# Kernel optimization log

Measured on AMD Instinct MI355X. Metric: run time of the kernel, lower is better.

Reference implementation:

```python
import jax, jax.numpy as jnp
import numpy as np

N_ITER = 25
TOP_G = 0.07
BOT_G = 0.07
N_MIX = 1.0  # n=1 -> top target is exactly global_target


def _conv(x, W, b, stride):
    # NCHW valid conv, matching torch Conv2d
    y = jax.lax.conv_general_dilated(
        x, W, (stride, stride), 'VALID',
        dimension_numbers=('NCHW', 'OIHW', 'NCHW'))
    return y + b[None, :, None, None]


def setup_inputs() -> dict:
    key = jax.random.key(0)
    ks = jax.random.split(key, 8)
    B = 2048
    x = jax.random.normal(ks[0], (B, 3, 32, 32), jnp.float32)
    global_target = jax.random.uniform(ks[1], (B, 10), jnp.float32)

    def he(k, shape, fan_in):
        return jax.random.normal(k, shape, jnp.float32) * (1.0 / np.sqrt(fan_in))

    W1 = he(ks[2], (64, 3, 5, 5), 3 * 25);    b1 = jnp.zeros((64,), jnp.float32)
    W2 = he(ks[3], (128, 64, 5, 5), 64 * 25); b2 = jnp.zeros((128,), jnp.float32)
    W3 = he(ks[4], (256, 128, 3, 3), 128 * 9); b3 = jnp.zeros((256,), jnp.float32)
    W4 = he(ks[5], (10, 1024), 1024);          b4 = jnp.zeros((10,), jnp.float32)
    return {"x": x, "global_target": global_target,
            "W1": W1, "b1": b1, "W2": W2, "b2": b2,
            "W3": W3, "b3": b3, "W4": W4, "b4": b4}


def reference(x, global_target, W1, b1, W2, b2, W3, b3, W4, b4):
    B = x.shape[0]
    # layer functions (wts[0..3] in the torch module)
    f1 = lambda z: jax.nn.relu(_conv(z, W1, b1, 2))                      # [B,64,14,14]
    f2 = lambda z: jax.nn.relu(_conv(z, W2, b2, 2))                      # [B,128,5,5]
    f3 = lambda z: jax.nn.relu(_conv(z, W3, b3, 2)).reshape(z.shape[0], -1)  # [B,1024]
    f4 = lambda z: z @ W4.T + b4                                         # [B,10]

    # compute_values: feedforward pass
    h1 = f1(x); h2 = f2(h1); h3 = f3(h2); h4 = f4(h3)
    # top target: n*global_target + (1-n)*h4  (n=1)
    t4 = N_MIX * global_target + (1.0 - N_MIX) * h4

    # compute_PC_targets: iterative inference.
    # p[1] = wts[0](targ[0]) = f1(x) is constant == h1, so eps1 = t1 - h1.
    def step(carry, _):
        t1, t2, t3, p2, p3, p4 = carry
        e1 = t1 - h1
        e2 = t2 - p2
        e3 = t3 - p3
        e4 = (t4 - jax.nn.softmax(p4, axis=1)) * 0.5
        # epsdfdt = vjp of next layer at current target, cotangent = next eps
        _, v2 = jax.vjp(f2, t1); (g1,) = v2(e2)
        _, v3 = jax.vjp(f3, t2); (g2,) = v3(e3)
        _, v4 = jax.vjp(f4, t3); (g3,) = v4(e4)
        t1 = t1 + TOP_G * (-e1) + BOT_G * g1
        t2 = t2 + TOP_G * (-e2) + BOT_G * g2
        t3 = t3 + TOP_G * (-e3) + BOT_G * g3
        # recompute predictions from updated targets
        p2 = f2(t1); p3 = f3(t2); p4 = f4(t3)
        return (t1, t2, t3, p2, p3, p4), None

    carry0 = (h1, h2, h3, h2, h3, h4)
    (t1, t2, t3, _, _, _), _ = jax.lax.scan(step, carry0, None, length=N_ITER)

    # return refined PC targets (targ[1..3]; targ[0]=x and targ[4]=global_target are fixed)
    return jnp.concatenate(
        [t1.reshape(B, -1), t2.reshape(B, -1), t3.reshape(B, -1)], axis=1)
```

## Files before the change

kernel.cpp:

```cpp
#include <hip/hip_runtime.h>
#include <hip/hip_bf16.h>

typedef __hip_bfloat16 bf16;
typedef __attribute__((ext_vector_type(8))) short short8v;
typedef __attribute__((ext_vector_type(4))) float float4v;


__device__ __forceinline__ float b2f(bf16 v) { return __bfloat162float(v); }
__device__ __forceinline__ bf16  f2b(float v) { return __float2bfloat16(v); }
__device__ __forceinline__ float blo(unsigned u) { return __uint_as_float(u << 16); }
__device__ __forceinline__ float bhi(unsigned u) { return __uint_as_float(u & 0xffff0000u); }
__device__ __forceinline__ unsigned short fbits(float v) {
  union { bf16 b; unsigned short u; } c; c.b = f2b(v); return c.u;
}
__device__ __forceinline__ float ubf(unsigned short u) {
  return __uint_as_float(((unsigned)u) << 16);
}
__device__ __forceinline__ void gld16(const void* g, void* l) {
  __builtin_amdgcn_global_load_lds((const unsigned int*)g, (unsigned int*)l, 16, 0, 0);
}

__global__ __launch_bounds__(256) void k_prep(
    const float* __restrict__ W1, const float* __restrict__ W2,
    const float* __restrict__ W3, float* __restrict__ W1t,
    short* __restrict__ W2f, short* __restrict__ W2u,
    short* __restrict__ W3m, short* __restrict__ W3u) {
  int i = blockIdx.x * 256 + threadIdx.x;
  if (i < 4800) {
    int oc = i / 75, k = i % 75;
    W1t[k * 64 + oc] = W1[i];
  }
  if (i < 204800) {
    int oc = i / 1600, k = i % 1600, ic = k / 25, tap = k % 25;
    float w = W2[i];
    unsigned short hi = fbits(w);
    unsigned short lo = fbits(w - ubf(hi));
    W2f[(tap * 128 + oc) * 64 + (ic ^ ((oc & 7) << 3))] = (short)hi;
    W2f[204800 + (tap * 128 + oc) * 64 + (ic ^ ((oc & 7) << 3))] = (short)lo;
    W2u[(tap * 64 + ic) * 128 + (oc ^ ((ic & 7) << 3))] = (short)hi;
  }
  if (i < 294912) {
    int oc = i / 1152, k = i % 1152, ic = k / 9, tap = k % 9;
    float w = W3[i];
    unsigned short hi = fbits(w);
    unsigned short lo = fbits(w - ubf(hi));
    W3m[(tap * 256 + oc) * 128 + (ic ^ ((oc & 7) << 3))] = (short)hi;
    W3m[294912 + (tap * 256 + oc) * 128 + (ic ^ ((oc & 7) << 3))] = (short)lo;
    W3u[(tap * 128 + ic) * 256 + (oc ^ ((ic & 7) << 3))] = (short)hi;
  }
}

__global__ __launch_bounds__(512, 1) void k_conv1s(
    const float* __restrict__ x, const float* __restrict__ W1t,
    const float* __restrict__ b1, bf16* __restrict__ h1T) {
  __shared__ float xs[480 * 66];
  __shared__ float ws[4800];
  int bt = blockIdx.x, oy = blockIdx.y;
  int tid = threadIdx.x, lane = tid & 63, w8 = tid >> 6;
  int wv = w8 & 3, h = w8 >> 2;
  for (int i = tid; i < 4800; i += 512) ws[i] = W1t[i];
#pragma unroll
  for (int r = 0; r < 15; ++r) {
    int idx = r * 512 + tid;
    int col = idx / 120, q = idx % 120;
    int ic = q / 40, rem = q % 40;
    float4 v = *(const float4*)(x + (size_t)(bt * 64 + col) * 3072 +
                                ic * 1024 + oy * 64 + rem * 4);
    float* d = xs + (ic * 160 + rem * 4) * 66 + col;
    d[0] = v.x;
    d[66] = v.y;
    d[132] = v.z;
    d[198] = v.w;
  }
  __syncthreads();
  int oc0 = wv * 16;
  float acc[7][16];
#pragma unroll
  for (int o = 0; o < 7; ++o)
#pragma unroll
    for (int j = 0; j < 16; ++j) acc[o][j] = b1[oc0 + j];
  for (int ic = 0; ic < 3; ++ic)
    for (int ky = 0; ky < 5; ++ky) {
#pragma unroll
      for (int kx = 0; kx < 5; ++kx) {
        const float* wp = ws + ((ic * 25 + ky * 5 + kx) << 6) + oc0;
        float4 w0 = *(const float4*)(wp);
        float4 w1 = *(const float4*)(wp + 4);
        float4 w2 = *(const float4*)(wp + 8);
        float4 w3 = *(const float4*)(wp + 12);
        const float* xr = xs + (ic * 160 + ky * 32 + kx) * 66 + lane;
        float xv[7];
#pragma unroll
        for (int o = 0; o < 7; ++o) xv[o] = xr[(2 * (h * 7 + o)) * 66];
#pragma unroll
        for (int o = 0; o < 7; ++o) {
          float e = xv[o];
          acc[o][0] += e * w0.x;  acc[o][1] += e * w0.y;
          acc[o][2] += e * w0.z;  acc[o][3] += e * w0.w;
          acc[o][4] += e * w1.x;  acc[o][5] += e * w1.y;
          acc[o][6] += e * w1.z;  acc[o][7] += e * w1.w;
          acc[o][8] += e * w2.x;  acc[o][9] += e * w2.y;
          acc[o][10] += e * w2.z; acc[o][11] += e * w2.w;
          acc[o][12] += e * w3.x; acc[o][13] += e * w3.y;
          acc[o][14] += e * w3.z; acc[o][15] += e * w3.w;
        }
      }
    }
#pragma unroll
  for (int o = 0; o < 7; ++o) {
    int pix = oy * 14 + h * 7 + o;
    size_t tbase = ((size_t)(pix * 32 + bt)) << 12;
#pragma unroll
    for (int q = 0; q < 4; ++q) {
      ushort4 pk;
      pk.x = fbits(fmaxf(acc[o][q * 4 + 0], 0.f));
      pk.y = fbits(fmaxf(acc[o][q * 4 + 1], 0.f));
      pk.z = fbits(fmaxf(acc[o][q * 4 + 2], 0.f));
      pk.w = fbits(fmaxf(acc[o][q * 4 + 3], 0.f));
      int ocr = oc0 + q * 4;
      size_t off = tbase + lane * 64 + (ocr ^ ((lane & 7) << 3));
      *(ushort4*)(h1T + off) = pk;
    }
  }
}

__global__ __launch_bounds__(256) void k_fwd2m(
    const bf16* __restrict__ in1, const short* __restrict__ W2f,
    const float* __restrict__ b2, bf16* __restrict__ p2T,
    const bf16* __restrict__ t2e, bf16* __restrict__ e2T, int einit) {
  __shared__ __align__(16) short As0[8192];
  __shared__ __align__(16) short As1[8192];
  __shared__ __align__(16) short Bs[2][4096];
  int bid = blockIdx.x;
  int j = bid >> 3;
  int cbp = (bid & 7) * 2 + (j & 1), pos = j >> 1;
  int cb0 = cbp * 2;
  int tid = threadIdx.x, lane = tid & 63, wv = tid >> 6;
  int oy = pos / 5, ox = pos % 5;
  float4v acc[2][2][4];
#pragma unroll
  for (int c = 0; c < 2; ++c)
#pragma unroll
    for (int m = 0; m < 2; ++m)
#pragma unroll
      for (int n = 0; n < 4; ++n) acc[c][m][n] = (float4v){0.f, 0.f, 0.f, 0.f};

  for (int tap = 0; tap < 25; ++tap) {
    int ky = tap / 5, kx = tap % 5;
    int ipix = (2 * oy + ky) * 14 + (2 * ox + kx);
    __syncthreads();
    {
      const uint4* bs0 = (const uint4*)(in1 + (((size_t)(ipix * 32 + cb0)) << 12));
      const uint4* bs1 = (const uint4*)(in1 + (((size_t)(ipix * 32 + cb0 + 1)) << 12));
      uint4* bd = (uint4*)Bs;
      gld16(&bs0[tid], &bd[tid]);
      gld16(&bs0[tid + 256], &bd[tid + 256]);
      gld16(&bs1[tid], &bd[tid + 512]);
      gld16(&bs1[tid + 256], &bd[tid + 768]);
      const uint4* ah = (const uint4*)(W2f + tap * 8192);
      const uint4* al = (const uint4*)(W2f + 204800 + tap * 8192);
      uint4* dh = (uint4*)As0;
      uint4* dl = (uint4*)As1;
#pragma unroll
      for (int p = 0; p < 4; ++p) {
        gld16(&ah[tid + p * 256], &dh[tid + p * 256]);
        gld16(&al[tid + p * 256], &dl[tid + p * 256]);
      }
    }
    __syncthreads();
#pragma unroll
    for (int ks = 0; ks < 2; ++ks) {
      int ic0 = ks * 32 + ((lane >> 4) << 3);
      short8v bfr[2][4];
#pragma unroll
      for (int c = 0; c < 2; ++c)
#pragma unroll
        for (int n = 0; n < 4; ++n) {
          int colv = n * 16 + (lane & 15);
          bfr[c][n] = *(const short8v*)(&Bs[c][0] + colv * 64 + (ic0 ^ ((colv & 7) << 3)));
        }
#pragma unroll
      for (int m = 0; m < 2; ++m) {
        int row = wv * 32 + m * 16 + (lane & 15);
        int aoff = row * 64 + (ic0 ^ ((row & 7) << 3));
        short8v ah = *(const short8v*)(As0 + aoff);
        short8v al = *(const short8v*)(As1 + aoff);
#pragma unroll
        for (int c = 0; c < 2; ++c)
#pragma unroll
          for (int n = 0; n < 4; ++n) {
            acc[c][m][n] = __builtin_amdgcn_mfma_f32_16x16x32_bf16(ah, bfr[c][n], acc[c][m][n], 0, 0, 0);
            acc[c][m][n] = __builtin_amdgcn_mfma_f32_16x16x32_bf16(al, bfr[c][n], acc[c][m][n], 0, 0, 0);
          }
      }
    }
  }
#pragma unroll
  for (int c = 0; c < 2; ++c) {
    size_t tb2 = ((size_t)(pos * 32 + cb0 + c)) << 13;
#pragma unroll
    for (int m = 0; m < 2; ++m) {
      int ocb = wv * 32 + m * 16 + ((lane >> 4) << 2);
      float4 bv = *(const float4*)(b2 + ocb);
#pragma unroll
      for (int n = 0; n < 4; ++n) {
        int colv = n * 16 + (lane & 15);
        ushort4 pk;
        pk.x = fbits(fmaxf(acc[c][m][n][0] + bv.x, 0.f));
        pk.y = fbits(fmaxf(acc[c][m][n][1] + bv.y, 0.f));
        pk.z = fbits(fmaxf(acc[c][m][n][2] + bv.z, 0.f));
        pk.w = fbits(fmaxf(acc[c][m][n][3] + bv.w, 0.f));
        size_t off = tb2 + colv * 128 + (ocb ^ ((colv & 7) << 3));
        *(ushort4*)(p2T + off) = pk;
        if (einit) {
          ushort4 z = {0, 0, 0, 0};
          *(ushort4*)(e2T + off) = z;
        } else {
          ushort4 tv = *(const ushort4*)(t2e + off);
          ushort4 ev;
          float p0, t0;
          p0 = ubf(pk.x); t0 = ubf(tv.x); ev.x = fbits(p0 > 0.f ? t0 - p0 : 0.f);
          p0 = ubf(pk.y); t0 = ubf(tv.y); ev.y = fbits(p0 > 0.f ? t0 - p0 : 0.f);
          p0 = ubf(pk.z); t0 = ubf(tv.z); ev.z = fbits(p0 > 0.f ? t0 - p0 : 0.f);
          p0 = ubf(pk.w); t0 = ubf(tv.w); ev.w = fbits(p0 > 0.f ? t0 - p0 : 0.f);
          *(ushort4*)(e2T + off) = ev;
        }
      }
    }
  }
}

__global__ __launch_bounds__(256) void k_upd1m(
    const bf16* __restrict__ e2T, const short* __restrict__ W2u,
    const bf16* __restrict__ h1T, const bf16* __restrict__ t1r,
    bf16* __restrict__ t1w) {
  __shared__ __align__(16) short As0[8192];
  __shared__ __align__(16) short Es[2][8192];
  int bid = blockIdx.x;
  int j = bid >> 3;
  int cbp = (bid & 7) * 2 + (j & 1), pix = j >> 1;
  int cb0 = cbp * 2;
  int tid = threadIdx.x, lane = tid & 63, wv = tid >> 6;
  int iy = pix / 14, ix = pix % 14;
  float4v acc[2][4];
#pragma unroll
  for (int c = 0; c < 2; ++c)
#pragma unroll
    for (int n = 0; n < 4; ++n) acc[c][n] = (float4v){0.f, 0.f, 0.f, 0.f};

  for (int ky = iy & 1; ky <= 4; ky += 2) {
    int oy = (iy - ky) >> 1;
    if (oy < 0 || oy > 4) continue;
    for (int kx = ix & 1; kx <= 4; kx += 2) {
      int ox = (ix - kx) >> 1;
      if (ox < 0 || ox > 4) continue;
      int erow = oy * 5 + ox, tap = ky * 5 + kx;
      __syncthreads();
      {
        const uint4* es0 = (const uint4*)(e2T + (((size_t)(erow * 32 + cb0)) << 13));
        const uint4* es1 = (const uint4*)(e2T + (((size_t)(erow * 32 + cb0 + 1)) << 13));
        uint4* ed = (uint4*)Es;
        const uint4* ah = (const uint4*)(W2u + tap * 8192);
        uint4* dh = (uint4*)As0;
#pragma unroll
        for (int p = 0; p < 4; ++p) {
          gld16(&es0[tid + p * 256], &ed[tid + p * 256]);
          gld16(&es1[tid + p * 256], &ed[tid + p * 256 + 1024]);
          gld16(&ah[tid + p * 256], &dh[tid + p * 256]);
        }
      }
      __syncthreads();
#pragma unroll
      for (int ks = 0; ks < 4; ++ks) {
        int oc0 = ks * 32 + ((lane >> 4) << 3);
        int row = wv * 16 + (lane & 15);
        int aoff = row * 128 + (oc0 ^ ((row & 7) << 3));
        short8v ah = *(const short8v*)(As0 + aoff);
#pragma unroll
        for (int c = 0; c < 2; ++c)
#pragma unroll
          for (int n = 0; n < 4; ++n) {
            int colv = n * 16 + (lane & 15);
            short8v ef = *(const short8v*)(&Es[c][0] + colv * 128 + (oc0 ^ ((colv & 7) << 3)));
            acc[c][n] = __builtin_amdgcn_mfma_f32_16x16x32_bf16(ah, ef, acc[c][n], 0, 0, 0);
          }
      }
    }
  }
  int icb = wv * 16 + ((lane >> 4) << 2);
#pragma unroll
  for (int c = 0; c < 2; ++c) {
    size_t tb1 = ((size_t)(pix * 32 + cb0 + c)) << 12;
#pragma unroll
    for (int n = 0; n < 4; ++n) {
      int colv = n * 16 + (lane & 15);
      size_t off = tb1 + colv * 64 + (icb ^ ((colv & 7) << 3));
      ushort4 tv = *(const ushort4*)(t1r + off);
      ushort4 hv = *(const ushort4*)(h1T + off);
      ushort4 rp;
      float t0, h0;
      t0 = ubf(tv.x); h0 = ubf(hv.x);
      rp.x = fbits(t0 - 0.07f * (t0 - h0) + 0.07f * acc[c][n][0]);
      t0 = ubf(tv.y); h0 = ubf(hv.y);
      rp.y = fbits(t0 - 0.07f * (t0 - h0) + 0.07f * acc[c][n][1]);
      t0 = ubf(tv.z); h0 = ubf(hv.z);
      rp.z = fbits(t0 - 0.07f * (t0 - h0) + 0.07f * acc[c][n][2]);
      t0 = ubf(tv.w); h0 = ubf(hv.w);
      rp.w = fbits(t0 - 0.07f * (t0 - h0) + 0.07f * acc[c][n][3]);
      *(ushort4*)(t1w + off) = rp;
    }
  }
}

__global__ __launch_bounds__(256) void k_fwd3m(
    const bf16* __restrict__ in2, const short* __restrict__ W3m,
    const float* __restrict__ b3, bf16* __restrict__ p3T,
    const bf16* __restrict__ t3e, bf16* __restrict__ e3T, int einit) {
  __shared__ __align__(16) short As0[8192];
  __shared__ __align__(16) short As1[8192];
  __shared__ __align__(16) short Bs[8192];
  int bid = blockIdx.x;
  int j = bid >> 3;
  int cb = (bid & 7) * 4 + (j & 3);
  int r = j >> 2;
  int pos = r & 3, och = r >> 2;
  int tid = threadIdx.x, lane = tid & 63, wv = tid >> 6;
  int oy = pos >> 1, ox = pos & 1;
  float4v acc[4];
#pragma unroll
  for (int n = 0; n < 4; ++n) acc[n] = (float4v){0.f, 0.f, 0.f, 0.f};

  for (int tap = 0; tap < 9; ++tap) {
    int ky = tap / 3, kx = tap % 3;
    int irow = (2 * oy + ky) * 5 + (2 * ox + kx);
    __syncthreads();
    {
      const uint4* bs = (const uint4*)(in2 + (((size_t)(irow * 32 + cb)) << 13));
      uint4* bd = (uint4*)Bs;
#pragma unroll
      for (int p = 0; p < 4; ++p) gld16(&bs[tid + p * 256], &bd[tid + p * 256]);
      const uint4* ah = (const uint4*)(W3m + ((size_t)tap * 256 + och * 64) * 128);
      const uint4* al = (const uint4*)(W3m + 294912 + ((size_t)tap * 256 + och * 64) * 128);
      uint4* dh = (uint4*)As0;
      uint4* dl = (uint4*)As1;
#pragma unroll
      for (int p = 0; p < 4; ++p) {
        gld16(&ah[tid + p * 256], &dh[tid + p * 256]);
        gld16(&al[tid + p * 256], &dl[tid + p * 256]);
      }
    }
    __syncthreads();
#pragma unroll
    for (int ks = 0; ks < 4; ++ks) {
      int ic0 = ks * 32 + ((lane >> 4) << 3);
      short8v bfr[4];
#pragma unroll
      for (int n = 0; n < 4; ++n) {
        int colv = n * 16 + (lane & 15);
        bfr[n] = *(const short8v*)(Bs + colv * 128 + (ic0 ^ ((colv & 7) << 3)));
      }
      int row = wv * 16 + (lane & 15);
      int aoff = row * 128 + (ic0 ^ ((row & 7) << 3));
      short8v ah = *(const short8v*)(As0 + aoff);
      short8v al = *(const short8v*)(As1 + aoff);
#pragma unroll
      for (int n = 0; n < 4; ++n) {
        acc[n] = __builtin_amdgcn_mfma_f32_16x16x32_bf16(ah, bfr[n], acc[n], 0, 0, 0);
        acc[n] = __builtin_amdgcn_mfma_f32_16x16x32_bf16(al, bfr[n], acc[n], 0, 0, 0);
      }
    }
  }
  size_t tb3 = ((size_t)(pos * 32 + cb)) << 14;
  int ocg = och * 64 + wv * 16 + ((lane >> 4) << 2);
  float4 bv = *(const float4*)(b3 + ocg);
#pragma unroll
  for (int n = 0; n < 4; ++n) {
    int colv = n * 16 + (lane & 15);
    ushort4 pk;
    pk.x = fbits(fmaxf(acc[n][0] + bv.x, 0.f));
    pk.y = fbits(fmaxf(acc[n][1] + bv.y, 0.f));
    pk.z = fbits(fmaxf(acc[n][2] + bv.z, 0.f));
    pk.w = fbits(fmaxf(acc[n][3] + bv.w, 0.f));
    size_t off = tb3 + colv * 256 + (ocg ^ ((colv & 7) << 3));
    *(ushort4*)(p3T + off) = pk;
    if (einit) {
      ushort4 z = {0, 0, 0, 0};
      *(ushort4*)(e3T + off) = z;
    } else {
      ushort4 tv = *(const ushort4*)(t3e + off);
      ushort4 ev;
      float p0, t0;
      p0 = ubf(pk.x); t0 = ubf(tv.x); ev.x = fbits(p0 > 0.f ? t0 - p0 : 0.f);
      p0 = ubf(pk.y); t0 = ubf(tv.y); ev.y = fbits(p0 > 0.f ? t0 - p0 : 0.f);
      p0 = ubf(pk.z); t0 = ubf(tv.z); ev.z = fbits(p0 > 0.f ? t0 - p0 : 0.f);
      p0 = ubf(pk.w); t0 = ubf(tv.w); ev.w = fbits(p0 > 0.f ? t0 - p0 : 0.f);
      *(ushort4*)(e3T + off) = ev;
    }
  }
}

__global__ __launch_bounds__(256) void k_upd2m(
    const bf16* __restrict__ e3T, const bf16* __restrict__ p2T,
    const short* __restrict__ W3u, const bf16* __restrict__ t2r,
    bf16* __restrict__ t2w) {
  __shared__ __align__(16) short Es[8192];
  __shared__ __align__(16) short As0[16384];
  int bid = blockIdx.x;
  int j = bid >> 3;
  int cb = (bid & 7) * 4 + (j & 3), pix = j >> 2;
  int tid = threadIdx.x, lane = tid & 63, wv = tid >> 6;
  int iy = pix / 5, ix = pix % 5;
  float4v acc[2][4];
#pragma unroll
  for (int m = 0; m < 2; ++m)
#pragma unroll
    for (int n = 0; n < 4; ++n) acc[m][n] = (float4v){0.f, 0.f, 0.f, 0.f};

  for (int ky = iy & 1; ky <= 2; ky += 2) {
    int oy = (iy - ky) >> 1;
    if (oy < 0 || oy > 1) continue;
    for (int kx = ix & 1; kx <= 2; kx += 2) {
      int ox = (ix - kx) >> 1;
      if (ox < 0 || ox > 1) continue;
      int erow = oy * 2 + ox, tap = ky * 3 + kx;
      for (int occ = 0; occ < 2; ++occ) {
        __syncthreads();
        {
          size_t tb = ((size_t)(erow * 32 + cb)) << 14;
          uint4* ed = (uint4*)Es;
#pragma unroll
          for (int p = 0; p < 4; ++p) {
            int fi = tid + p * 256;
            int colr = fi >> 4, q = fi & 15;
            size_t g = tb + colr * 256 + occ * 128 + q * 8;
            gld16(e3T + g, &ed[fi]);
          }
          uint4* dh = (uint4*)As0;
#pragma unroll
          for (int p = 0; p < 8; ++p) {
            int fi = tid + p * 256;
            int icr = fi >> 4, q = fi & 15;
            size_t srcoff = ((size_t)(tap * 128 + icr)) * 256 + occ * 128 + q * 8;
            gld16(W3u + srcoff, &dh[fi]);
          }
        }
        __syncthreads();
#pragma unroll
        for (int ks = 0; ks < 4; ++ks) {
          int oc0 = ks * 32 + ((lane >> 4) << 3);
          short8v efr[4];
#pragma unroll
          for (int n = 0; n < 4; ++n) {
            int colv = n * 16 + (lane & 15);
            efr[n] = *(const short8v*)(Es + colv * 128 + (oc0 ^ ((colv & 7) << 3)));
          }
#pragma unroll
          for (int m = 0; m < 2; ++m) {
            int icr = wv * 32 + m * 16 + (lane & 15);
            int aoff = icr * 128 + (oc0 ^ ((icr & 7) << 3));
            short8v ah = *(const short8v*)(As0 + aoff);
#pragma unroll
            for (int n = 0; n < 4; ++n) {
              acc[m][n] = __builtin_amdgcn_mfma_f32_16x16x32_bf16(ah, efr[n], acc[m][n], 0, 0, 0);
            }
          }
        }
      }
    }
  }
  size_t tb2 = ((size_t)(pix * 32 + cb)) << 13;
#pragma unroll
  for (int m = 0; m < 2; ++m) {
    int icr = wv * 32 + m * 16 + ((lane >> 4) << 2);
#pragma unroll
    for (int n = 0; n < 4; ++n) {
      int colv = n * 16 + (lane & 15);
      size_t off = tb2 + colv * 128 + (icr ^ ((colv & 7) << 3));
      ushort4 tv = *(const ushort4*)(t2r + off);
      ushort4 pv = *(const ushort4*)(p2T + off);
      ushort4 rp;
      float t0, p0;
      t0 = ubf(tv.x); p0 = ubf(pv.x);
      rp.x = fbits(t0 - 0.07f * (t0 - p0) + 0.07f * acc[m][n][0]);
      t0 = ubf(tv.y); p0 = ubf(pv.y);
      rp.y = fbits(t0 - 0.07f * (t0 - p0) + 0.07f * acc[m][n][1]);
      t0 = ubf(tv.z); p0 = ubf(pv.z);
      rp.z = fbits(t0 - 0.07f * (t0 - p0) + 0.07f * acc[m][n][2]);
      t0 = ubf(tv.w); p0 = ubf(pv.w);
      rp.w = fbits(t0 - 0.07f * (t0 - p0) + 0.07f * acc[m][n][3]);
      *(ushort4*)(t2w + off) = rp;
    }
  }
}

__global__ __launch_bounds__(256) void k_fu3(
    const float* __restrict__ gt, const float* __restrict__ W4,
    const float* __restrict__ b4, const bf16* __restrict__ p3T,
    const bf16* __restrict__ t3r, bf16* __restrict__ t3w) {
  __shared__ __align__(16) float w4s[10240];
  int tid = threadIdx.x;
  {
    const uint4* wsrc = (const uint4*)W4;
    uint4* wdst = (uint4*)w4s;
#pragma unroll
    for (int k = 0; k < 10; ++k) gld16(&wsrc[tid + k * 256], &wdst[tid + k * 256]);
  }
  __syncthreads();
  int c = blockIdx.x * 8 + (tid >> 5);
  int cb = c >> 6, colL = c & 63, subk = tid & 31;
  int pos = subk & 3, ch0 = (subk >> 2) * 32;
  int xc = (colL & 7) << 3;
  size_t boff = (((size_t)(pos * 32 + cb)) << 14) + colL * 256 + ch0;
  const bf16* trd = t3r + boff;
  const bf16* pb = p3T + boff;
  uint4 tq[4];
#pragma unroll
  for (int q = 0; q < 4; ++q) tq[q] = *(const uint4*)(trd + q * 8);
  float acc[10] = {};
#pragma unroll
  for (int q = 0; q < 4; ++q) {
    unsigned wds[4] = {tq[q].x, tq[q].y, tq[q].z, tq[q].w};
    int chb = (ch0 + q * 8) ^ xc;
#pragma unroll
    for (int h = 0; h < 4; ++h) {
      float v0 = blo(wds[h]), v1 = bhi(wds[h]);
      int k0 = (chb + 2 * h) * 4 + pos;
#pragma unroll
      for (int o = 0; o < 10; ++o)
        acc[o] += v0 * w4s[o * 1024 + k0] + v1 * w4s[o * 1024 + k0 + 4];
    }
  }
#pragma unroll
  for (int off = 16; off > 0; off >>= 1)
#pragma unroll
    for (int o = 0; o < 10; ++o) acc[o] += __shfl_xor(acc[o], off, 32);
  float pv[10], m = -1e30f;
#pragma unroll
  for (int o = 0; o < 10; ++o) {
    pv[o] = acc[o] + b4[o];
    m = fmaxf(m, pv[o]);
  }
  float s = 0.f;
#pragma unroll
  for (int o = 0; o < 10; ++o) {
    pv[o] = __expf(pv[o] - m);
    s += pv[o];
  }
  float inv = 1.f / s;
  float e4[10];
#pragma unroll
  for (int o = 0; o < 10; ++o)
    e4[o] = (gt[(size_t)c * 10 + o] - pv[o] * inv) * 0.5f;
  bf16* tb = t3w + boff;
#pragma unroll
  for (int q = 0; q < 4; ++q) {
    uint4 pq = *(const uint4*)(pb + q * 8);
    unsigned tw[4] = {tq[q].x, tq[q].y, tq[q].z, tq[q].w};
    unsigned pw[4] = {pq.x, pq.y, pq.z, pq.w};
    int chb = (ch0 + q * 8) ^ xc;
    unsigned ro[4];
#pragma unroll
    for (int h = 0; h < 4; ++h) {
      int k0 = (chb + 2 * h) * 4 + pos;
      float g0 = 0.f, g1 = 0.f;
#pragma unroll
      for (int o = 0; o < 10; ++o) {
        g0 += e4[o] * w4s[o * 1024 + k0];
        g1 += e4[o] * w4s[o * 1024 + k0 + 4];
      }
      float t0 = blo(tw[h]), p0 = blo(pw[h]);
      float t1 = bhi(tw[h]), p1 = bhi(pw[h]);
      float r0 = t0 - 0.07f * (t0 - p0) + 0.07f * g0;
      float r1 = t1 - 0.07f * (t1 - p1) + 0.07f * g1;
      ro[h] = (unsigned)fbits(r0) | ((unsigned)fbits(r1) << 16);
    }
    uint4 rv = {ro[0], ro[1], ro[2], ro[3]};
    *(uint4*)(tb + q * 8) = rv;
  }
}

__global__ __launch_bounds__(256) void k_tr1(
    const bf16* __restrict__ t1T, float* __restrict__ out) {
  __shared__ short lds[2 * 64 * 224];
  int cb = blockIdx.x, c0 = blockIdx.y * 2;
  int tid = threadIdx.x;
  for (int i = tid; i < 3136; i += 256) {
    int pix = i >> 4, q = i & 15;
    int colL = q >> 3, chb = (q & 7) << 3;
    int col = c0 + colL;
    uint4 v = *(const uint4*)(t1T + (((size_t)(pix * 32 + cb)) << 12) + col * 64 + chb);
    int icb = chb ^ ((col & 7) << 3);
    int posX = pix ^ (((icb >> 3) & 7) << 2);
    short* d = lds + (colL * 64 + icb) * 224 + posX;
    const short* vs = (const short*)&v;
#pragma unroll
    for (int j = 0; j < 8; ++j) d[j * 224] = vs[j];
  }
  __syncthreads();
  for (int i = tid; i < 6272; i += 256) {
    int colL = i / 3136, m = i % 3136;
    int ic = m / 49, pp = m % 49;
    int posX = (pp * 4) ^ (((ic >> 3) & 7) << 2);
    const short* s = lds + (colL * 64 + ic) * 224 + posX;
    float4 o;
    o.x = ubf((unsigned short)s[0]);
    o.y = ubf((unsigned short)s[1]);
    o.z = ubf((unsigned short)s[2]);
    o.w = ubf((unsigned short)s[3]);
    *(float4*)(out + ((size_t)(cb * 64 + c0 + colL)) * 16768 + m * 4) = o;
  }
}

__global__ __launch_bounds__(256) void k_tr2(
    const bf16* __restrict__ t2T, float* __restrict__ out) {
  __shared__ short lds[4 * 128 * 32];
  int cb = blockIdx.x, c0 = blockIdx.y * 4;
  int tid = threadIdx.x;
  for (int i = tid; i < 1600; i += 256) {
    int pos = i >> 6, q = i & 63;
    int colL = q >> 4, chb = (q & 15) << 3;
    int col = c0 + colL;
    uint4 v = *(const uint4*)(t2T + (((size_t)(pos * 32 + cb)) << 13) + col * 128 + chb);
    int ocb = chb ^ ((col & 7) << 3);
    int posX = pos ^ (((ocb >> 3) & 7) << 2);
    short* d = lds + (colL * 128 + ocb) * 32 + posX;
    const short* vs = (const short*)&v;
#pragma unroll
    for (int j = 0; j < 8; ++j) d[j * 32] = vs[j];
  }
  __syncthreads();
  for (int i = tid; i < 3200; i += 256) {
    int colL = i / 800, m = i % 800;
    int f0 = m * 4;
    float4 o;
    float* po = &o.x;
#pragma unroll
    for (int t = 0; t < 4; ++t) {
      int f = f0 + t;
      int oc = f / 25, pos = f % 25;
      int posX = pos ^ (((oc >> 3) & 7) << 2);
      po[t] = ubf((unsigned short)lds[(colL * 128 + oc) * 32 + posX]);
    }
    *(float4*)(out + ((size_t)(cb * 64 + c0 + colL)) * 16768 + 12544 + f0) = o;
  }
}

__global__ __launch_bounds__(256) void k_tr3(
    const bf16* __restrict__ t3T, float* __restrict__ out) {
  int tid = threadIdx.x;
  int sample = blockIdx.x * 8 + (tid >> 5);
  int cb = sample >> 6, col = sample & 63;
  int chb = (tid & 31) << 3;
  int icb = chb ^ ((col & 7) << 3);
  uint4 v[4];
#pragma unroll
  for (int pos = 0; pos < 4; ++pos)
    v[pos] = *(const uint4*)(t3T + (((size_t)(pos * 32 + cb)) << 14) + col * 256 + chb);
  const unsigned short* s0 = (const unsigned short*)&v[0];
  const unsigned short* s1 = (const unsigned short*)&v[1];
  const unsigned short* s2 = (const unsigned short*)&v[2];
  const unsigned short* s3 = (const unsigned short*)&v[3];
  float* ob = out + (size_t)sample * 16768 + 15744 + icb * 4;
#pragma unroll
  for (int j = 0; j < 8; ++j) {
    float4 o;
    o.x = ubf(s0[j]);
    o.y = ubf(s1[j]);
    o.z = ubf(s2[j]);
    o.w = ubf(s3[j]);
    *(float4*)(ob + j * 4) = o;
  }
}

extern "C" void kernel_launch(void* const* d_in, const int* in_sizes, int n_in,
                              void* d_out, int out_size, void* d_ws,
                              size_t ws_size, hipStream_t stream) {
  const float* x  = (const float*)d_in[0];
  const float* gt = (const float*)d_in[1];
  const float* W1 = (const float*)d_in[2];
  const float* b1 = (const float*)d_in[3];
  const float* W2 = (const float*)d_in[4];
  const float* b2 = (const float*)d_in[5];
  const float* W3 = (const float*)d_in[6];
  const float* b3 = (const float*)d_in[7];
  const float* W4 = (const float*)d_in[8];
  const float* b4 = (const float*)d_in[9];
  float* out = (float*)d_out;

  bf16* h1T = (bf16*)d_ws;
  bf16* t1T = h1T + 25690112ull;
  bf16* t2T = t1T + 25690112ull;
  bf16* p2T = t2T + 6553600ull;
  bf16* t3T = p2T + 6553600ull;
  bf16* p3T = t3T + 2097152ull;
  float* p4f = (float*)(p3T + 2097152ull);
  float* W1t = p4f + 20480;
  short* W3m = (short*)(W1t + 4800);
  short* W3u = W3m + 589824;
  short* W2f = W3u + 589824;
  short* W2u = W2f + 409600;
  bf16* e2T = (bf16*)out;
  bf16* e3T = e2T + 6553600ull;

  dim3 blk(256);

  k_prep<<<1152, blk, 0, stream>>>(W1, W2, W3, W1t, W2f, W2u, W3m, W3u);
  k_conv1s<<<dim3(32, 14), dim3(512), 0, stream>>>(x, W1t, b1, h1T);
  k_fwd2m<<<400, blk, 0, stream>>>(h1T, W2f, b2, p2T, p2T, e2T, 1);
  k_fwd3m<<<512, blk, 0, stream>>>(p2T, W3m, b3, p3T, p3T, e3T, 1);

  for (int it = 0; it < 25; ++it) {
    const bf16* t1r = (it == 0) ? h1T : t1T;
    const bf16* t2r = (it == 0) ? p2T : t2T;
    const bf16* t3r = (it == 0) ? p3T : t3T;
    k_upd1m<<<3136, blk, 0, stream>>>(e2T, W2u, h1T, t1r, t1T);
    k_upd2m<<<800, blk, 0, stream>>>(e3T, p2T, W3u, t2r, t2T);
    k_fu3<<<256, blk, 0, stream>>>(gt, W4, b4, p3T, t3r, t3T);
    if (it < 24) {
      k_fwd2m<<<400, blk, 0, stream>>>(t1T, W2f, b2, p2T, t2T, e2T, 0);
      k_fwd3m<<<512, blk, 0, stream>>>(t2T, W3m, b3, p3T, t3T, e3T, 0);
    }
  }
  k_tr1<<<dim3(32, 32), blk, 0, stream>>>(t1T, out);
  k_tr2<<<dim3(32, 16), blk, 0, stream>>>(t2T, out);
  k_tr3<<<256, blk, 0, stream>>>(t3T, out);
}
```

Measured before the change: 3.648 ms.

## Merge per-iteration update and forward kernels into two multi-role launches

```diff
diff --git a/kernel.cpp b/kernel.cpp
--- a/kernel.cpp
+++ b/kernel.cpp
@@ -124,18 +124,19 @@
   }
 }
 
-__global__ __launch_bounds__(256) void k_fwd2m(
-    const bf16* __restrict__ in1, const short* __restrict__ W2f,
-    const float* __restrict__ b2, bf16* __restrict__ p2T,
-    const bf16* __restrict__ t2e, bf16* __restrict__ e2T, int einit) {
-  __shared__ __align__(16) short As0[8192];
-  __shared__ __align__(16) short As1[8192];
-  __shared__ __align__(16) short Bs[2][4096];
-  int bid = blockIdx.x;
+
+__device__ __forceinline__ void fwd2_body(
+    int bid, int tid, short* s, const bf16* __restrict__ in1,
+    const short* __restrict__ W2f, const float* __restrict__ b2,
+    bf16* __restrict__ p2T, const bf16* __restrict__ t2e,
+    bf16* __restrict__ e2T, int einit) {
+  short* As0 = s;
+  short* As1 = s + 8192;
+  short* Bs = s + 16384;
   int j = bid >> 3;
   int cbp = (bid & 7) * 2 + (j & 1), pos = j >> 1;
   int cb0 = cbp * 2;
-  int tid = threadIdx.x, lane = tid & 63, wv = tid >> 6;
+  int lane = tid & 63, wv = tid >> 6;
   int oy = pos / 5, ox = pos % 5;
   float4v acc[2][2][4];
 #pragma unroll
@@ -177,7 +178,7 @@
 #pragma unroll
         for (int n = 0; n < 4; ++n) {
           int colv = n * 16 + (lane & 15);
-          bfr[c][n] = *(const short8v*)(&Bs[c][0] + colv * 64 + (ic0 ^ ((colv & 7) << 3)));
+          bfr[c][n] = *(const short8v*)(Bs + c * 4096 + colv * 64 + (ic0 ^ ((colv & 7) << 3)));
         }
 #pragma unroll
       for (int m = 0; m < 2; ++m) {
@@ -230,101 +231,19 @@
   }
 }
 
-__global__ __launch_bounds__(256) void k_upd1m(
-    const bf16* __restrict__ e2T, const short* __restrict__ W2u,
-    const bf16* __restrict__ h1T, const bf16* __restrict__ t1r,
-    bf16* __restrict__ t1w) {
-  __shared__ __align__(16) short As0[8192];
-  __shared__ __align__(16) short Es[2][8192];
-  int bid = blockIdx.x;
-  int j = bid >> 3;
-  int cbp = (bid & 7) * 2 + (j & 1), pix = j >> 1;
-  int cb0 = cbp * 2;
-  int tid = threadIdx.x, lane = tid & 63, wv = tid >> 6;
-  int iy = pix / 14, ix = pix % 14;
-  float4v acc[2][4];
-#pragma unroll
-  for (int c = 0; c < 2; ++c)
-#pragma unroll
-    for (int n = 0; n < 4; ++n) acc[c][n] = (float4v){0.f, 0.f, 0.f, 0.f};
-
-  for (int ky = iy & 1; ky <= 4; ky += 2) {
-    int oy = (iy - ky) >> 1;
-    if (oy < 0 || oy > 4) continue;
-    for (int kx = ix & 1; kx <= 4; kx += 2) {
-      int ox = (ix - kx) >> 1;
-      if (ox < 0 || ox > 4) continue;
-      int erow = oy * 5 + ox, tap = ky * 5 + kx;
-      __syncthreads();
-      {
-        const uint4* es0 = (const uint4*)(e2T + (((size_t)(erow * 32 + cb0)) << 13));
-        const uint4* es1 = (const uint4*)(e2T + (((size_t)(erow * 32 + cb0 + 1)) << 13));
-        uint4* ed = (uint4*)Es;
-        const uint4* ah = (const uint4*)(W2u + tap * 8192);
-        uint4* dh = (uint4*)As0;
-#pragma unroll
-        for (int p = 0; p < 4; ++p) {
-          gld16(&es0[tid + p * 256], &ed[tid + p * 256]);
-          gld16(&es1[tid + p * 256], &ed[tid + p * 256 + 1024]);
-          gld16(&ah[tid + p * 256], &dh[tid + p * 256]);
-        }
-      }
-      __syncthreads();
-#pragma unroll
-      for (int ks = 0; ks < 4; ++ks) {
-        int oc0 = ks * 32 + ((lane >> 4) << 3);
-        int row = wv * 16 + (lane & 15);
-        int aoff = row * 128 + (oc0 ^ ((row & 7) << 3));
-        short8v ah = *(const short8v*)(As0 + aoff);
-#pragma unroll
-        for (int c = 0; c < 2; ++c)
-#pragma unroll
-          for (int n = 0; n < 4; ++n) {
-            int colv = n * 16 + (lane & 15);
-            short8v ef = *(const short8v*)(&Es[c][0] + colv * 128 + (oc0 ^ ((colv & 7) << 3)));
-            acc[c][n] = __builtin_amdgcn_mfma_f32_16x16x32_bf16(ah, ef, acc[c][n], 0, 0, 0);
-          }
-      }
-    }
-  }
-  int icb = wv * 16 + ((lane >> 4) << 2);
-#pragma unroll
-  for (int c = 0; c < 2; ++c) {
-    size_t tb1 = ((size_t)(pix * 32 + cb0 + c)) << 12;
-#pragma unroll
-    for (int n = 0; n < 4; ++n) {
-      int colv = n * 16 + (lane & 15);
-      size_t off = tb1 + colv * 64 + (icb ^ ((colv & 7) << 3));
-      ushort4 tv = *(const ushort4*)(t1r + off);
-      ushort4 hv = *(const ushort4*)(h1T + off);
-      ushort4 rp;
-      float t0, h0;
-      t0 = ubf(tv.x); h0 = ubf(hv.x);
-      rp.x = fbits(t0 - 0.07f * (t0 - h0) + 0.07f * acc[c][n][0]);
-      t0 = ubf(tv.y); h0 = ubf(hv.y);
-      rp.y = fbits(t0 - 0.07f * (t0 - h0) + 0.07f * acc[c][n][1]);
-      t0 = ubf(tv.z); h0 = ubf(hv.z);
-      rp.z = fbits(t0 - 0.07f * (t0 - h0) + 0.07f * acc[c][n][2]);
-      t0 = ubf(tv.w); h0 = ubf(hv.w);
-      rp.w = fbits(t0 - 0.07f * (t0 - h0) + 0.07f * acc[c][n][3]);
-      *(ushort4*)(t1w + off) = rp;
-    }
-  }
-}
-
-__global__ __launch_bounds__(256) void k_fwd3m(
-    const bf16* __restrict__ in2, const short* __restrict__ W3m,
-    const float* __restrict__ b3, bf16* __restrict__ p3T,
-    const bf16* __restrict__ t3e, bf16* __restrict__ e3T, int einit) {
-  __shared__ __align__(16) short As0[8192];
-  __shared__ __align__(16) short As1[8192];
-  __shared__ __align__(16) short Bs[8192];
-  int bid = blockIdx.x;
+__device__ __forceinline__ void fwd3_body(
+    int bid, int tid, short* s, const bf16* __restrict__ in2,
+    const short* __restrict__ W3m, const float* __restrict__ b3,
+    bf16* __restrict__ p3T, const bf16* __restrict__ t3e,
+    bf16* __restrict__ e3T, int einit) {
+  short* As0 = s;
+  short* As1 = s + 8192;
+  short* Bs = s + 16384;
   int j = bid >> 3;
   int cb = (bid & 7) * 4 + (j & 3);
   int r = j >> 2;
   int pos = r & 3, och = r >> 2;
-  int tid = threadIdx.x, lane = tid & 63, wv = tid >> 6;
+  int lane = tid & 63, wv = tid >> 6;
   int oy = pos >> 1, ox = pos & 1;
   float4v acc[4];
 #pragma unroll
@@ -399,16 +318,96 @@
   }
 }
 
-__global__ __launch_bounds__(256) void k_upd2m(
-    const bf16* __restrict__ e3T, const bf16* __restrict__ p2T,
-    const short* __restrict__ W3u, const bf16* __restrict__ t2r,
-    bf16* __restrict__ t2w) {
-  __shared__ __align__(16) short Es[8192];
-  __shared__ __align__(16) short As0[16384];
-  int bid = blockIdx.x;
+__device__ __forceinline__ void upd1_body(
+    int bid, int tid, short* s, const bf16* __restrict__ e2T,
+    const short* __restrict__ W2u, const bf16* __restrict__ h1T,
+    const bf16* __restrict__ t1r, bf16* __restrict__ t1w) {
+  short* As0 = s;
+  short* Es = s + 8192;
+  int j = bid >> 3;
+  int cbp = (bid & 7) * 2 + (j & 1), pix = j >> 1;
+  int cb0 = cbp * 2;
+  int lane = tid & 63, wv = tid >> 6;
+  int iy = pix / 14, ix = pix % 14;
+  float4v acc[2][4];
+#pragma unroll
+  for (int c = 0; c < 2; ++c)
+#pragma unroll
+    for (int n = 0; n < 4; ++n) acc[c][n] = (float4v){0.f, 0.f, 0.f, 0.f};
+
+  for (int ky = iy & 1; ky <= 4; ky += 2) {
+    int oy = (iy - ky) >> 1;
+    if (oy < 0 || oy > 4) continue;
+    for (int kx = ix & 1; kx <= 4; kx += 2) {
+      int ox = (ix - kx) >> 1;
+      if (ox < 0 || ox > 4) continue;
+      int erow = oy * 5 + ox, tap = ky * 5 + kx;
+      __syncthreads();
+      {
+        const uint4* es0 = (const uint4*)(e2T + (((size_t)(erow * 32 + cb0)) << 13));
+        const uint4* es1 = (const uint4*)(e2T + (((size_t)(erow * 32 + cb0 + 1)) << 13));
+        uint4* ed = (uint4*)Es;
+        const uint4* ah = (const uint4*)(W2u + tap * 8192);
+        uint4* dh = (uint4*)As0;
+#pragma unroll
+        for (int p = 0; p < 4; ++p) {
+          gld16(&es0[tid + p * 256], &ed[tid + p * 256]);
+          gld16(&es1[tid + p * 256], &ed[tid + p * 256 + 1024]);
+          gld16(&ah[tid + p * 256], &dh[tid + p * 256]);
+        }
+      }
+      __syncthreads();
+#pragma unroll
+      for (int ks = 0; ks < 4; ++ks) {
+        int oc0 = ks * 32 + ((lane >> 4) << 3);
+        int row = wv * 16 + (lane & 15);
+        int aoff = row * 128 + (oc0 ^ ((row & 7) << 3));
+        short8v ah = *(const short8v*)(As0 + aoff);
+#pragma unroll
+        for (int c = 0; c < 2; ++c)
+#pragma unroll
+          for (int n = 0; n < 4; ++n) {
+            int colv = n * 16 + (lane & 15);
+            short8v ef = *(const short8v*)(Es + c * 8192 + colv * 128 + (oc0 ^ ((colv & 7) << 3)));
+            acc[c][n] = __builtin_amdgcn_mfma_f32_16x16x32_bf16(ah, ef, acc[c][n], 0, 0, 0);
+          }
+      }
+    }
+  }
+  int icb = wv * 16 + ((lane >> 4) << 2);
+#pragma unroll
+  for (int c = 0; c < 2; ++c) {
+    size_t tb1 = ((size_t)(pix * 32 + cb0 + c)) << 12;
+#pragma unroll
+    for (int n = 0; n < 4; ++n) {
+      int colv = n * 16 + (lane & 15);
+      size_t off = tb1 + colv * 64 + (icb ^ ((colv & 7) << 3));
+      ushort4 tv = *(const ushort4*)(t1r + off);
+      ushort4 hv = *(const ushort4*)(h1T + off);
+      ushort4 rp;
+      float t0, h0;
+      t0 = ubf(tv.x); h0 = ubf(hv.x);
+      rp.x = fbits(t0 - 0.07f * (t0 - h0) + 0.07f * acc[c][n][0]);
+      t0 = ubf(tv.y); h0 = ubf(hv.y);
+      rp.y = fbits(t0 - 0.07f * (t0 - h0) + 0.07f * acc[c][n][1]);
+      t0 = ubf(tv.z); h0 = ubf(hv.z);
+      rp.z = fbits(t0 - 0.07f * (t0 - h0) + 0.07f * acc[c][n][2]);
+      t0 = ubf(tv.w); h0 = ubf(hv.w);
+      rp.w = fbits(t0 - 0.07f * (t0 - h0) + 0.07f * acc[c][n][3]);
+      *(ushort4*)(t1w + off) = rp;
+    }
+  }
+}
+
+__device__ __forceinline__ void upd2_body(
+    int bid, int tid, short* s, const bf16* __restrict__ e3T,
+    const bf16* __restrict__ p2T, const short* __restrict__ W3u,
+    const bf16* __restrict__ t2r, bf16* __restrict__ t2w) {
+  short* Es = s;
+  short* As0 = s + 8192;
   int j = bid >> 3;
   int cb = (bid & 7) * 4 + (j & 3), pix = j >> 2;
-  int tid = threadIdx.x, lane = tid & 63, wv = tid >> 6;
+  int lane = tid & 63, wv = tid >> 6;
   int iy = pix / 5, ix = pix % 5;
   float4v acc[2][4];
 #pragma unroll
@@ -493,12 +492,12 @@
   }
 }
 
-__global__ __launch_bounds__(256) void k_fu3(
-    const float* __restrict__ gt, const float* __restrict__ W4,
-    const float* __restrict__ b4, const bf16* __restrict__ p3T,
-    const bf16* __restrict__ t3r, bf16* __restrict__ t3w) {
-  __shared__ __align__(16) float w4s[10240];
-  int tid = threadIdx.x;
+__device__ __forceinline__ void fu3_body(
+    int bid, int tid, short* s, const float* __restrict__ gt,
+    const float* __restrict__ W4, const float* __restrict__ b4,
+    const bf16* __restrict__ p3T, const bf16* __restrict__ t3r,
+    bf16* __restrict__ t3w) {
+  float* w4s = (float*)s;
   {
     const uint4* wsrc = (const uint4*)W4;
     uint4* wdst = (uint4*)w4s;
@@ -506,7 +505,7 @@
     for (int k = 0; k < 10; ++k) gld16(&wsrc[tid + k * 256], &wdst[tid + k * 256]);
   }
   __syncthreads();
-  int c = blockIdx.x * 8 + (tid >> 5);
+  int c = bid * 8 + (tid >> 5);
   int cb = c >> 6, colL = c & 63, subk = tid & 31;
   int pos = subk & 3, ch0 = (subk >> 2) * 32;
   int xc = (colL & 7) << 3;
@@ -540,13 +539,13 @@
     pv[o] = acc[o] + b4[o];
     m = fmaxf(m, pv[o]);
   }
-  float s = 0.f;
+  float sum = 0.f;
 #pragma unroll
   for (int o = 0; o < 10; ++o) {
     pv[o] = __expf(pv[o] - m);
-    s += pv[o];
-  }
-  float inv = 1.f / s;
+    sum += pv[o];
+  }
+  float inv = 1.f / sum;
   float e4[10];
 #pragma unroll
   for (int o = 0; o < 10; ++o)
@@ -576,6 +575,59 @@
     }
     uint4 rv = {ro[0], ro[1], ro[2], ro[3]};
     *(uint4*)(tb + q * 8) = rv;
+  }
+}
+
+
+__global__ __launch_bounds__(256) void k_fwd2m(
+    const bf16* __restrict__ in1, const short* __restrict__ W2f,
+    const float* __restrict__ b2, bf16* __restrict__ p2T,
+    const bf16* __restrict__ t2e, bf16* __restrict__ e2T, int einit) {
+  __shared__ __align__(16) short smem[24576];
+  fwd2_body(blockIdx.x, threadIdx.x, smem, in1, W2f, b2, p2T, t2e, e2T, einit);
+}
+
+__global__ __launch_bounds__(256) void k_fwd3m(
+    const bf16* __restrict__ in2, const short* __restrict__ W3m,
+    const float* __restrict__ b3, bf16* __restrict__ p3T,
+    const bf16* __restrict__ t3e, bf16* __restrict__ e3T, int einit) {
+  __shared__ __align__(16) short smem[24576];
+  fwd3_body(blockIdx.x, threadIdx.x, smem, in2, W3m, b3, p3T, t3e, e3T, einit);
+}
+
+__global__ __launch_bounds__(256) void k_updall(
+    const bf16* __restrict__ e2T, const short* __restrict__ W2u,
+    const bf16* __restrict__ h1T, const bf16* __restrict__ t1r,
+    bf16* __restrict__ t1w, const bf16* __restrict__ e3T,
+    const bf16* __restrict__ p2T, const short* __restrict__ W3u,
+    const bf16* __restrict__ t2r, bf16* __restrict__ t2w,
+    const float* __restrict__ gt, const float* __restrict__ W4,
+    const float* __restrict__ b4, const bf16* __restrict__ p3T,
+    const bf16* __restrict__ t3r, bf16* __restrict__ t3w) {
+  __shared__ __align__(16) short smem[24576];
+  int bid = blockIdx.x, tid = threadIdx.x;
+  if (bid < 3136) {
+    upd1_body(bid, tid, smem, e2T, W2u, h1T, t1r, t1w);
+  } else if (bid < 3936) {
+    upd2_body(bid - 3136, tid, smem, e3T, p2T, W3u, t2r, t2w);
+  } else {
+    fu3_body(bid - 3936, tid, smem, gt, W4, b4, p3T, t3r, t3w);
+  }
+}
+
+__global__ __launch_bounds__(256) void k_fwdall(
+    const bf16* __restrict__ t1T, const short* __restrict__ W2f,
+    const float* __restrict__ b2, bf16* __restrict__ p2T,
+    const bf16* __restrict__ t2T, bf16* __restrict__ e2T,
+    const short* __restrict__ W3m, const float* __restrict__ b3,
+    bf16* __restrict__ p3T, const bf16* __restrict__ t3T,
+    bf16* __restrict__ e3T) {
+  __shared__ __align__(16) short smem[24576];
+  int bid = blockIdx.x, tid = threadIdx.x;
+  if (bid < 400) {
+    fwd2_body(bid, tid, smem, t1T, W2f, b2, p2T, t2T, e2T, 0);
+  } else {
+    fwd3_body(bid - 400, tid, smem, t2T, W3m, b3, p3T, t3T, e3T, 0);
   }
 }
 
@@ -713,12 +765,12 @@
     const bf16* t1r = (it == 0) ? h1T : t1T;
     const bf16* t2r = (it == 0) ? p2T : t2T;
     const bf16* t3r = (it == 0) ? p3T : t3T;
-    k_upd1m<<<3136, blk, 0, stream>>>(e2T, W2u, h1T, t1r, t1T);
-    k_upd2m<<<800, blk, 0, stream>>>(e3T, p2T, W3u, t2r, t2T);
-    k_fu3<<<256, blk, 0, stream>>>(gt, W4, b4, p3T, t3r, t3T);
+    k_updall<<<4192, blk, 0, stream>>>(e2T, W2u, h1T, t1r, t1T,
+                                       e3T, p2T, W3u, t2r, t2T,
+                                       gt, W4, b4, p3T, t3r, t3T);
     if (it < 24) {
-      k_fwd2m<<<400, blk, 0, stream>>>(t1T, W2f, b2, p2T, t2T, e2T, 0);
-      k_fwd3m<<<512, blk, 0, stream>>>(t2T, W3m, b3, p3T, t3T, e3T, 0);
+      k_fwdall<<<912, blk, 0, stream>>>(t1T, W2f, b2, p2T, t2T, e2T,
+                                        W3m, b3, p3T, t3T, e3T);
     }
   }
   k_tr1<<<dim3(32, 32), blk, 0, stream>>>(t1T, out);
```

Result: slower. 3.856 ms (+5.7%).
